# Kernel tuning notes

Hardware: AMD Instinct MI355X
Metric: run time of the kernel (lower is better)

## Reference

```python
import jax, jax.numpy as jnp
import numpy as np

WS = (2, 7, 7)   # window size (D,H,W)
SS = (1, 3, 3)   # shift size
NUM_HEADS = 12
EPS = 1e-5


def _window_partition(x, ws):
    B, D, H, W, C = x.shape
    x = x.reshape(B, D // ws[0], ws[0], H // ws[1], ws[1], W // ws[2], ws[2], C)
    return x.transpose(0, 1, 3, 5, 2, 4, 6, 7).reshape(-1, ws[0] * ws[1] * ws[2], C)


def _window_reverse(win, ws, B, D, H, W):
    x = win.reshape(B, D // ws[0], H // ws[1], W // ws[2], ws[0], ws[1], ws[2], -1)
    return x.transpose(0, 1, 4, 2, 5, 3, 6, 7).reshape(B, D, H, W, -1)


def _relative_position_index(ws):
    coords = np.stack(np.meshgrid(np.arange(ws[0]), np.arange(ws[1]), np.arange(ws[2]), indexing='ij'))
    cf = coords.reshape(3, -1)
    rel = (cf[:, :, None] - cf[:, None, :]).transpose(1, 2, 0)
    rel[:, :, 0] += ws[0] - 1
    rel[:, :, 1] += ws[1] - 1
    rel[:, :, 2] += ws[2] - 1
    rel[:, :, 0] *= (2 * ws[1] - 1) * (2 * ws[2] - 1)
    rel[:, :, 1] *= 2 * ws[2] - 1
    return rel.sum(-1)  # (N, N)


def _compute_mask(D, H, W, ws, ss):
    img = np.zeros((1, D, H, W, 1), dtype=np.float32)
    def sl(w, s):
        return [slice(-w), slice(-w, -s), slice(-s, None)] if s > 0 else [slice(None)]
    cnt = 0
    for d in sl(ws[0], ss[0]):
        for h in sl(ws[1], ss[1]):
            for w in sl(ws[2], ss[2]):
                img[:, d, h, w, :] = cnt
                cnt += 1
    # numpy window partition
    x = img.reshape(1, D // ws[0], ws[0], H // ws[1], ws[1], W // ws[2], ws[2], 1)
    mw = x.transpose(0, 1, 3, 5, 2, 4, 6, 7).reshape(-1, ws[0] * ws[1] * ws[2])
    diff = mw[:, None, :] - mw[:, :, None]
    return np.where(diff != 0, -100.0, 0.0).astype(np.float32)  # (nW, N, N)


def _layernorm(x, w, b):
    m = x.mean(-1, keepdims=True)
    v = ((x - m) ** 2).mean(-1, keepdims=True)
    return (x - m) * jax.lax.rsqrt(v + EPS) * w + b


def setup_inputs() -> dict:
    key = jax.random.key(0)
    ks = jax.random.split(key, 16)
    C = 384
    Hd = 4 * C
    nB = (2 * WS[0] - 1) * (2 * WS[1] - 1) * (2 * WS[2] - 1)
    s = lambda k, shape, f=0.02: jax.random.normal(k, shape, jnp.float32) * f
    return {
        'x': jax.random.normal(ks[0], (2, 8, 56, 56, C), jnp.float32),
        'norm1_w': jnp.ones((C,), jnp.float32), 'norm1_b': jnp.zeros((C,), jnp.float32),
        'qkv_w': s(ks[1], (3 * C, C)), 'qkv_b': jnp.zeros((3 * C,), jnp.float32),
        'rpb_table': s(ks[2], (nB, NUM_HEADS)),
        'proj_w': s(ks[3], (C, C)), 'proj_b': jnp.zeros((C,), jnp.float32),
        'norm2_w': jnp.ones((C,), jnp.float32), 'norm2_b': jnp.zeros((C,), jnp.float32),
        'fc1_w': s(ks[4], (Hd, C)), 'fc1_b': jnp.zeros((Hd,), jnp.float32),
        'fc2_w': s(ks[5], (C, Hd)), 'fc2_b': jnp.zeros((C,), jnp.float32),
    }


def reference(x, norm1_w, norm1_b, qkv_w, qkv_b, rpb_table, proj_w, proj_b,
              norm2_w, norm2_b, fc1_w, fc1_b, fc2_w, fc2_b):
    B, D, H, W, C = x.shape
    h = NUM_HEADS
    hd = C // h
    scale = hd ** -0.5
    N = WS[0] * WS[1] * WS[2]

    shortcut = x
    xn = _layernorm(x, norm1_w, norm1_b)
    # dims are exact multiples of window size -> no padding needed
    shifted = jnp.roll(xn, shift=(-SS[0], -SS[1], -SS[2]), axis=(1, 2, 3))
    xw = _window_partition(shifted, WS)  # (B_, N, C)
    B_ = xw.shape[0]

    qkv = (xw @ qkv_w.T + qkv_b).reshape(B_, N, 3, h, hd).transpose(2, 0, 3, 1, 4)
    q, k, v = qkv[0], qkv[1], qkv[2]  # (B_, h, N, hd)
    attn = jnp.einsum('bhnd,bhmd->bhnm', q * scale, k)

    rel_idx = _relative_position_index(WS)  # static numpy (N, N)
    bias = rpb_table[rel_idx.reshape(-1)].reshape(N, N, h).transpose(2, 0, 1)
    attn = attn + bias[None]

    mask = jnp.asarray(_compute_mask(D, H, W, WS, SS))  # (nW, N, N)
    nW = mask.shape[0]
    attn = attn.reshape(B_ // nW, nW, h, N, N) + mask[None, :, None]
    attn = jax.nn.softmax(attn.reshape(B_, h, N, N), axis=-1)

    out = jnp.einsum('bhnm,bhmd->bhnd', attn, v).transpose(0, 2, 1, 3).reshape(B_, N, C)
    out = out @ proj_w.T + proj_b

    xr = _window_reverse(out, WS, B, D, H, W)
    xr = jnp.roll(xr, shift=SS, axis=(1, 2, 3))
    x = shortcut + xr  # drop_path = 0

    y = _layernorm(x, norm2_w, norm2_b)
    y = jax.nn.gelu(y @ fc1_w.T + fc1_b, approximate=False) @ fc2_w.T + fc2_b
    return x + y
```

## Files before the change

### kernel.cpp

```cpp
#include <hip/hip_runtime.h>
#include <hip/hip_bf16.h>

typedef __hip_bfloat16 bf16;
typedef __attribute__((ext_vector_type(8))) short bf16x8;
typedef __attribute__((ext_vector_type(4))) float f32x4;

__device__ __forceinline__ float tof(bf16 v) { return __bfloat162float(v); }
__device__ __forceinline__ float ldf(const float* p) { return *p; }
__device__ __forceinline__ float ldf(const bf16* p) { return __bfloat162float(*p); }
__device__ __forceinline__ void stf(float* p, float v) { *p = v; }
__device__ __forceinline__ void stf(bf16* p, float v) { *p = __float2bfloat16(v); }
__device__ __forceinline__ short bfbits(float v) {
    return (short)__builtin_bit_cast(unsigned short, __float2bfloat16(v));
}

__device__ __forceinline__ void gl2lds16(const void* g, void* l) {
    __builtin_amdgcn_global_load_lds((const __attribute__((address_space(1))) void*)g,
                                     (__attribute__((address_space(3))) void*)l, 16, 0, 0);
}

constexpr int TOK   = 50176;
constexpr int CCH   = 384;
constexpr int NELEM = TOK * CCH;
constexpr int BT_N  = 8 * 12 * 98 * 112;

__device__ __forceinline__ int remap_row(int m) {
    int b_ = m / 98, n = m % 98;
    int b = b_ >> 8, wrem = b_ & 255;
    int dw = wrem >> 6, hw = (wrem >> 3) & 7, wwi = wrem & 7;
    int zd = n / 49, r = n % 49, zh = r / 7, zw = r % 7;
    int d = ((dw * 2 + zd) + 1) & 7;
    int h = hw * 7 + zh + 3; if (h >= 56) h -= 56;
    int w = wwi * 7 + zw + 3; if (w >= 56) w -= 56;
    return ((b * 8 + d) * 56 + h) * 56 + w;
}

template <bool SRC_INPUT>
__global__ __launch_bounds__(256) void ln_kernel(const void* __restrict__ srcv,
                                                 const float* __restrict__ g,
                                                 const float* __restrict__ be,
                                                 bf16* __restrict__ dst) {
    int wave = threadIdx.x >> 6, lane = threadIdx.x & 63;
    int t = blockIdx.x * 4 + wave;
    int srcRow = SRC_INPUT ? remap_row(t) : t;
    float v[6];
    float s = 0.f, ss = 0.f;
#pragma unroll
    for (int j = 0; j < 6; ++j) {
        size_t idx = (size_t)srcRow * CCH + lane + 64 * j;
        v[j] = SRC_INPUT ? ((const float*)srcv)[idx] : tof(((const bf16*)srcv)[idx]);
        s += v[j];
        ss += v[j] * v[j];
    }
#pragma unroll
    for (int off = 32; off; off >>= 1) {
        s  += __shfl_xor(s, off, 64);
        ss += __shfl_xor(ss, off, 64);
    }
    float mean = s * (1.f / 384.f);
    float var  = ss * (1.f / 384.f) - mean * mean;
    float rstd = rsqrtf(var + 1e-5f);
    bf16* q = dst + (size_t)t * CCH;
#pragma unroll
    for (int j = 0; j < 6; ++j) {
        int c = lane + 64 * j;
        stf(q + c, (v[j] - mean) * rstd * g[c] + be[c]);
    }
}

__global__ __launch_bounds__(256) void cvt_split(const float* __restrict__ w,
                                                 bf16* __restrict__ hi,
                                                 bf16* __restrict__ lo, int n) {
    int i = blockIdx.x * 256 + threadIdx.x;
    if (i >= n) return;
    float f = w[i];
    bf16 h = __float2bfloat16(f);
    hi[i] = h;
    lo[i] = __float2bfloat16(f - __bfloat162float(h));
}

__global__ __launch_bounds__(256) void bias_precomp(const float* __restrict__ rpb,
                                                    float* __restrict__ table) {
    int bid = blockIdx.x;
    int cls = bid / 12, head = bid % 12;
    int cd = (cls >> 2) & 1, ch = (cls >> 1) & 1, cw = cls & 1;
    for (int e = threadIdx.x; e < 98 * 112; e += 256) {
        int i = e / 112, j = e % 112;
        float v;
        if (j >= 98) {
            v = -1e30f;
        } else {
            int di = i / 49, ri = i % 49, hi = ri / 7, wi = ri % 7;
            int dj = j / 49, rj = j % 49, hj = rj / 7, wj = rj % 7;
            int idx = (di - dj + 1) * 169 + (hi - hj + 6) * 13 + (wi - wj + 6);
            v = rpb[(size_t)idx * 12 + head];
            int ci = (cd ? (1 + di) : 0) * 9 + (ch ? (hi < 4 ? 1 : 2) : 0) * 3 +
                     (cw ? (wi < 4 ? 1 : 2) : 0);
            int cj = (cd ? (1 + dj) : 0) * 9 + (ch ? (hj < 4 ? 1 : 2) : 0) * 3 +
                     (cw ? (wj < 4 ? 1 : 2) : 0);
            if (ci != cj) v -= 100.f;
        }
        table[(size_t)bid * 98 * 112 + e] = v;
    }
}

template <int MODE, typename CT, typename XT>
__global__ __launch_bounds__(256, 2) void gemm_mfma(const bf16* __restrict__ A, int lda,
                                                    const bf16* __restrict__ Bh,
                                                    const bf16* __restrict__ Bl, int ldb,
                                                    const float* __restrict__ bias,
                                                    CT* __restrict__ Cc, int ldc,
                                                    const XT* __restrict__ Xres,
                                                    int M, int K) {
    __shared__ short As[8192];
    __shared__ short Bhs[8192];
    __shared__ short Bls[8192];
    const int tid  = threadIdx.x;
    const int lane = tid & 63;
    const int wv   = tid >> 6;
    const int wm   = wv >> 1, wn = wv & 1;
    const int nwg  = gridDim.x * gridDim.y;
    const int orig = blockIdx.y * gridDim.x + blockIdx.x;
    const int q8 = nwg >> 3, r8 = nwg & 7;
    const int xcd = orig & 7, slot = orig >> 3;
    const int work = (xcd < r8) ? xcd * (q8 + 1) + slot
                                : r8 * (q8 + 1) + (xcd - r8) * q8 + slot;
    const int bm = (work / gridDim.x) * 128, bn = (work % gridDim.x) * 128;
    const int kb = lane >> 4, r15 = lane & 15;

    f32x4 acc[4][4] = {};

    for (int k0 = 0; k0 < K; k0 += 64) {
#pragma unroll
        for (int p = 0; p < 4; ++p) {
            const int i    = p * 256 + tid;
            const int kbb  = i >> 7;
            const int rs   = i & 127;
            const int row  = rs ^ (kbb << 1);
            const int koff = k0 + kbb * 8;
            int mrow = bm + row; if (mrow >= M) mrow = M - 1;
            const int lslot = (p * 256 + (wv << 6)) * 8;
            gl2lds16(A  + (size_t)mrow * lda + koff, &As[lslot]);
            gl2lds16(Bh + (size_t)(bn + row) * ldb + koff, &Bhs[lslot]);
            gl2lds16(Bl + (size_t)(bn + row) * ldb + koff, &Bls[lslot]);
        }
        __syncthreads();

#pragma unroll
        for (int ks = 0; ks < 2; ++ks) {
            const int kg = ks * 4 + kb;
            bf16x8 af[4];
#pragma unroll
            for (int im = 0; im < 4; ++im) {
                const int row = wm * 64 + im * 16 + r15;
                af[im] = *(const bf16x8*)&As[(kg * 128 + (row ^ (kg << 1))) * 8];
            }
#pragma unroll
            for (int in = 0; in < 4; ++in) {
                const int col = wn * 64 + in * 16 + r15;
                const int sl  = (kg * 128 + (col ^ (kg << 1))) * 8;
                const bf16x8 bh = *(const bf16x8*)&Bhs[sl];
                const bf16x8 bl = *(const bf16x8*)&Bls[sl];
#pragma unroll
                for (int im = 0; im < 4; ++im) {
                    acc[im][in] = __builtin_amdgcn_mfma_f32_16x16x32_bf16(af[im], bh, acc[im][in], 0, 0, 0);
                    acc[im][in] = __builtin_amdgcn_mfma_f32_16x16x32_bf16(af[im], bl, acc[im][in], 0, 0, 0);
                }
            }
        }
        __syncthreads();
    }

#pragma unroll
    for (int im = 0; im < 4; ++im) {
        const int mb = bm + wm * 64 + im * 16 + (lane >> 4) * 4;
#pragma unroll
        for (int in = 0; in < 4; ++in) {
            const int c = bn + wn * 64 + in * 16 + r15;
            const float bv = bias[c];
#pragma unroll
            for (int r = 0; r < 4; ++r) {
                const int m = mb + r;
                if (m >= M) continue;
                float v = acc[im][in][r] + bv;
                if (MODE == 0) {
                    stf(Cc + (size_t)m * ldc + c, v);
                } else if (MODE == 1) {
                    size_t xi = (size_t)remap_row(m) * ldc + c;
                    stf(Cc + xi, ldf(Xres + xi) + v);
                } else if (MODE == 2) {
                    stf(Cc + (size_t)m * ldc + c,
                        0.5f * v * (1.f + erff(v * 0.70710678118654752f)));
                } else {
                    size_t xi = (size_t)m * ldc + c;
                    stf(Cc + xi, ldf(Xres + xi) + v);
                }
            }
        }
    }
}

__global__ __launch_bounds__(64) void attn_kernel(const bf16* __restrict__ qkv,
                                                  const float* __restrict__ bt,
                                                  bf16* __restrict__ outw, int gbase) {
    __shared__ short Vs[112 * 32];
    __shared__ short Ps[16 * 128];
    const int bid  = blockIdx.x;
    const int head = bid % 12;
    const int brel = bid / 12;
    const int babs = gbase + brel;
    const int lane = threadIdx.x;
    const int g = lane >> 4, c15 = lane & 15;

    const size_t qbase = (size_t)brel * 98 * 1152 + head * 32;

#pragma unroll
    for (int it = 0; it < 7; ++it) {
        int c = it * 64 + lane;
        int j = c >> 2, e0 = (c & 3) * 8;
        int jc = j < 98 ? j : 97;
        *(bf16x8*)&Vs[j * 32 + e0] =
            *(const bf16x8*)(qkv + qbase + (size_t)jc * 1152 + 768 + e0);
    }
    if (lane < 32) {
        int i = lane >> 1, half = lane & 1;
        int pb = (14 + half) ^ (i & 7);
        *(bf16x8*)&Ps[i * 128 + pb * 8] = bf16x8{0, 0, 0, 0, 0, 0, 0, 0};
    }

    bf16x8 qf[7], kf[7];
#pragma unroll
    for (int t7 = 0; t7 < 7; ++t7) {
        int qi = t7 * 16 + c15; if (qi > 97) qi = 97;
        const bf16* rp = qkv + qbase + (size_t)qi * 1152 + g * 8;
        qf[t7] = *(const bf16x8*)rp;
        kf[t7] = *(const bf16x8*)(rp + 384);
    }
    __syncthreads();

    bf16x8 vb[4][2];
#pragma unroll
    for (int kb = 0; kb < 4; ++kb)
#pragma unroll
        for (int t = 0; t < 2; ++t) {
            bf16x8 f;
#pragma unroll
            for (int e = 0; e < 8; ++e) {
                int j = kb * 32 + g * 8 + e;
                int jv = j < 112 ? j : 111;
                f[e] = Vs[jv * 32 + t * 16 + c15];
            }
            vb[kb][t] = f;
        }

    const int cls = ((((babs >> 6) & 3) == 3) ? 4 : 0) |
                    ((((babs >> 3) & 7) == 7) ? 2 : 0) |
                    (((babs & 7) == 7) ? 1 : 0);
    const float* btb = bt + (size_t)(cls * 12 + head) * 98 * 112;
    const float scale = 0.17677669529663687f;

#pragma unroll 1
    for (int it = 0; it < 7; ++it) {
        f32x4 s[7];
#pragma unroll
        for (int jt = 0; jt < 7; ++jt)
            s[jt] = __builtin_amdgcn_mfma_f32_16x16x32_bf16(qf[it], kf[jt],
                                                            f32x4{0, 0, 0, 0}, 0, 0, 0);
#pragma unroll
        for (int jt = 0; jt < 7; ++jt)
#pragma unroll
            for (int r = 0; r < 4; ++r) {
                int i = it * 16 + g * 4 + r; if (i > 97) i = 97;
                s[jt][r] = fmaf(s[jt][r], scale, btb[i * 112 + jt * 16 + c15]);
            }
        float mx[4], inv[4];
#pragma unroll
        for (int r = 0; r < 4; ++r) {
            float m = s[0][r];
#pragma unroll
            for (int jt = 1; jt < 7; ++jt) m = fmaxf(m, s[jt][r]);
#pragma unroll
            for (int off = 8; off; off >>= 1) m = fmaxf(m, __shfl_xor(m, off, 64));
            mx[r] = m;
        }
#pragma unroll
        for (int jt = 0; jt < 7; ++jt)
#pragma unroll
            for (int r = 0; r < 4; ++r) s[jt][r] = __expf(s[jt][r] - mx[r]);
#pragma unroll
        for (int r = 0; r < 4; ++r) {
            float t = 0.f;
#pragma unroll
            for (int jt = 0; jt < 7; ++jt) t += s[jt][r];
#pragma unroll
            for (int off = 8; off; off >>= 1) t += __shfl_xor(t, off, 64);
            inv[r] = 1.f / t;
        }
#pragma unroll
        for (int jt = 0; jt < 7; ++jt)
#pragma unroll
            for (int r = 0; r < 4; ++r) {
                int i = g * 4 + r;
                int j = jt * 16 + c15;
                int pj = ((((j >> 3) ^ (i & 7)) << 3)) | (j & 7);
                Ps[i * 128 + pj] = bfbits(s[jt][r]);
            }
        f32x4 o[2] = {f32x4{0, 0, 0, 0}, f32x4{0, 0, 0, 0}};
#pragma unroll
        for (int kb = 0; kb < 4; ++kb) {
            int pb = (kb * 4 + g) ^ (c15 & 7);
            bf16x8 pa = *(const bf16x8*)&Ps[c15 * 128 + pb * 8];
#pragma unroll
            for (int t = 0; t < 2; ++t)
                o[t] = __builtin_amdgcn_mfma_f32_16x16x32_bf16(pa, vb[kb][t], o[t], 0, 0, 0);
        }
#pragma unroll
        for (int t = 0; t < 2; ++t)
#pragma unroll
            for (int r = 0; r < 4; ++r) {
                int i = it * 16 + g * 4 + r;
                if (i < 98)
                    stf(outw + ((size_t)babs * 98 + i) * 384 + head * 32 + t * 16 + c15,
                        o[t][r] * inv[r]);
            }
    }
}

extern "C" void kernel_launch(void* const* d_in, const int* in_sizes, int n_in,
                              void* d_out, int out_size, void* d_ws, size_t ws_size,
                              hipStream_t stream) {
    const float* x      = (const float*)d_in[0];
    const float* n1w    = (const float*)d_in[1];
    const float* n1b    = (const float*)d_in[2];
    const float* qkv_w  = (const float*)d_in[3];
    const float* qkv_b  = (const float*)d_in[4];
    const float* rpb    = (const float*)d_in[5];
    const float* proj_w = (const float*)d_in[6];
    const float* proj_b = (const float*)d_in[7];
    const float* n2w    = (const float*)d_in[8];
    const float* n2b    = (const float*)d_in[9];
    const float* fc1_w  = (const float*)d_in[10];
    const float* fc1_b  = (const float*)d_in[11];
    const float* fc2_w  = (const float*)d_in[12];
    const float* fc2_b  = (const float*)d_in[13];

    bf16*  aout = (bf16*)d_out;
    float* btab = (float*)((char*)d_out + (size_t)NELEM * 2);
    bf16*  xn2  = (bf16*)((char*)d_out + (size_t)NELEM * 2);
    float* fout = (float*)d_out;

    constexpr int QKV_WN  = 1152 * 384;
    constexpr int PROJ_WN = 384 * 384;
    constexpr int FC1_WN  = 1536 * 384;
    constexpr int FC2_WN  = 384 * 1536;
    bf16* qh   = (bf16*)d_ws;
    bf16* ql   = qh  + QKV_WN;
    bf16* ph   = ql  + QKV_WN;
    bf16* pl   = ph  + PROJ_WN;
    bf16* f1h  = pl  + PROJ_WN;
    bf16* f1l  = f1h + FC1_WN;
    bf16* f2h  = f1l + FC1_WN;
    bf16* f2l  = f2h + FC2_WN;
    bf16* rA   = f2l + FC2_WN;
    bf16* rC   = rA + (size_t)NELEM;
    size_t used    = (size_t)((char*)rC - (char*)d_ws);
    size_t rCbytes = (ws_size > used) ? ws_size - used : 0;

    cvt_split<<<(QKV_WN  + 255) / 256, 256, 0, stream>>>(qkv_w,  qh,  ql,  QKV_WN);
    cvt_split<<<(PROJ_WN + 255) / 256, 256, 0, stream>>>(proj_w, ph,  pl,  PROJ_WN);
    cvt_split<<<(FC1_WN  + 255) / 256, 256, 0, stream>>>(fc1_w,  f1h, f1l, FC1_WN);
    cvt_split<<<(FC2_WN  + 255) / 256, 256, 0, stream>>>(fc2_w,  f2h, f2l, FC2_WN);
    bias_precomp<<<96, 256, 0, stream>>>(rpb, btab);

    int W = 512;
    while (W > 1 && (size_t)W * 98 * 1152 * 2 > rCbytes) W >>= 1;
    int nqg = 512 / W;
    int ngm = 1;
    while (ngm < 1024 && (size_t)(TOK / ngm) * 1536 * 2 > rCbytes) ngm <<= 1;
    int Mt = TOK / ngm;

    dim3 blk(256);

    ln_kernel<true><<<dim3(TOK / 4), blk, 0, stream>>>(x, n1w, n1b, rA);
    for (int g = 0; g < nqg; ++g) {
        int Mg = W * 98;
        gemm_mfma<0, bf16, float><<<dim3(1152 / 128, (Mg + 127) / 128), blk, 0, stream>>>(
            rA + (size_t)g * Mg * 384, 384, qh, ql, 384, qkv_b,
            rC, 1152, (const float*)nullptr, Mg, 384);
        attn_kernel<<<dim3(W * 12), dim3(64), 0, stream>>>(rC, btab, aout, g * W);
    }
    gemm_mfma<1, bf16, float><<<dim3(384 / 128, TOK / 128), blk, 0, stream>>>(
        aout, 384, ph, pl, 384, proj_b, rA, 384, x, TOK, 384);
    ln_kernel<false><<<dim3(TOK / 4), blk, 0, stream>>>(rA, n2w, n2b, xn2);
    for (int g = 0; g < ngm; ++g) {
        size_t off = (size_t)g * Mt * 384;
        gemm_mfma<2, bf16, float><<<dim3(1536 / 128, (Mt + 127) / 128), blk, 0, stream>>>(
            xn2 + off, 384, f1h, f1l, 384, fc1_b, rC, 1536, (const float*)nullptr, Mt, 384);
        gemm_mfma<4, float, bf16><<<dim3(384 / 128, (Mt + 127) / 128), blk, 0, stream>>>(
            rC, 1536, f2h, f2l, 1536, fc2_b, fout + off, 384, rA + off, Mt, 1536);
    }
}
```

Before: 1.196 ms.

## Double-buffer GEMM LDS tiles with BK=32 and use tanh-form GELU

The GEMM main loop now splits the LDS tiles into two 32-wide K buffers. It issues the global-to-LDS loads for the next K slice before running the MFMAs on the current one, so memory latency overlaps compute and one barrier per step is dropped. Separately, the fused GELU epilogue replaces the exact erf with a tanh approximation built from __expf and a hardware reciprocal. That makes the epilogue cheaper but departs slightly from the exact-erf GELU the reference specifies.

```diff
diff --git a/kernel.cpp b/kernel.cpp
--- a/kernel.cpp
+++ b/kernel.cpp
@@ -112,9 +112,9 @@
                                                     CT* __restrict__ Cc, int ldc,
                                                     const XT* __restrict__ Xres,
                                                     int M, int K) {
-    __shared__ short As[8192];
-    __shared__ short Bhs[8192];
-    __shared__ short Bls[8192];
+    __shared__ short As[2][4096];
+    __shared__ short Bhs[2][4096];
+    __shared__ short Bls[2][4096];
     const int tid  = threadIdx.x;
     const int lane = tid & 63;
     const int wv   = tid >> 6;
@@ -130,46 +130,55 @@
 
     f32x4 acc[4][4] = {};
 
-    for (int k0 = 0; k0 < K; k0 += 64) {
-#pragma unroll
-        for (int p = 0; p < 4; ++p) {
-            const int i    = p * 256 + tid;
-            const int kbb  = i >> 7;
-            const int rs   = i & 127;
-            const int row  = rs ^ (kbb << 1);
-            const int koff = k0 + kbb * 8;
-            int mrow = bm + row; if (mrow >= M) mrow = M - 1;
-            const int lslot = (p * 256 + (wv << 6)) * 8;
-            gl2lds16(A  + (size_t)mrow * lda + koff, &As[lslot]);
-            gl2lds16(Bh + (size_t)(bn + row) * ldb + koff, &Bhs[lslot]);
-            gl2lds16(Bl + (size_t)(bn + row) * ldb + koff, &Bls[lslot]);
+    const int i0   = tid, i1 = 256 + tid;
+    const int kbb0 = i0 >> 7, kbb1 = i1 >> 7;
+    const int row0 = (i0 & 127) ^ (kbb0 << 1);
+    const int row1 = (i1 & 127) ^ (kbb1 << 1);
+    int mrow0 = bm + row0; if (mrow0 >= M) mrow0 = M - 1;
+    int mrow1 = bm + row1; if (mrow1 >= M) mrow1 = M - 1;
+    const int ls0 = (0 * 256 + (wv << 6)) * 8;
+    const int ls1 = (1 * 256 + (wv << 6)) * 8;
+
+#define STAGE(buf, k0)                                                              \
+    do {                                                                            \
+        gl2lds16(A  + (size_t)mrow0 * lda + (k0) + kbb0 * 8, &As[buf][ls0]);        \
+        gl2lds16(Bh + (size_t)(bn + row0) * ldb + (k0) + kbb0 * 8, &Bhs[buf][ls0]); \
+        gl2lds16(Bl + (size_t)(bn + row0) * ldb + (k0) + kbb0 * 8, &Bls[buf][ls0]); \
+        gl2lds16(A  + (size_t)mrow1 * lda + (k0) + kbb1 * 8, &As[buf][ls1]);        \
+        gl2lds16(Bh + (size_t)(bn + row1) * ldb + (k0) + kbb1 * 8, &Bhs[buf][ls1]); \
+        gl2lds16(Bl + (size_t)(bn + row1) * ldb + (k0) + kbb1 * 8, &Bls[buf][ls1]); \
+    } while (0)
+
+    STAGE(0, 0);
+    __syncthreads();
+
+    const int nk = K >> 5;
+    int cur = 0;
+    for (int t = 0; t < nk; ++t) {
+        if (t + 1 < nk) STAGE(cur ^ 1, (t + 1) * 32);
+
+        bf16x8 af[4];
+#pragma unroll
+        for (int im = 0; im < 4; ++im) {
+            const int row = wm * 64 + im * 16 + r15;
+            af[im] = *(const bf16x8*)&As[cur][(kb * 128 + (row ^ (kb << 1))) * 8];
+        }
+#pragma unroll
+        for (int in = 0; in < 4; ++in) {
+            const int col = wn * 64 + in * 16 + r15;
+            const int sl  = (kb * 128 + (col ^ (kb << 1))) * 8;
+            const bf16x8 bh = *(const bf16x8*)&Bhs[cur][sl];
+            const bf16x8 bl = *(const bf16x8*)&Bls[cur][sl];
+#pragma unroll
+            for (int im = 0; im < 4; ++im) {
+                acc[im][in] = __builtin_amdgcn_mfma_f32_16x16x32_bf16(af[im], bh, acc[im][in], 0, 0, 0);
+                acc[im][in] = __builtin_amdgcn_mfma_f32_16x16x32_bf16(af[im], bl, acc[im][in], 0, 0, 0);
+            }
         }
         __syncthreads();
-
-#pragma unroll
-        for (int ks = 0; ks < 2; ++ks) {
-            const int kg = ks * 4 + kb;
-            bf16x8 af[4];
-#pragma unroll
-            for (int im = 0; im < 4; ++im) {
-                const int row = wm * 64 + im * 16 + r15;
-                af[im] = *(const bf16x8*)&As[(kg * 128 + (row ^ (kg << 1))) * 8];
-            }
-#pragma unroll
-            for (int in = 0; in < 4; ++in) {
-                const int col = wn * 64 + in * 16 + r15;
-                const int sl  = (kg * 128 + (col ^ (kg << 1))) * 8;
-                const bf16x8 bh = *(const bf16x8*)&Bhs[sl];
-                const bf16x8 bl = *(const bf16x8*)&Bls[sl];
-#pragma unroll
-                for (int im = 0; im < 4; ++im) {
-                    acc[im][in] = __builtin_amdgcn_mfma_f32_16x16x32_bf16(af[im], bh, acc[im][in], 0, 0, 0);
-                    acc[im][in] = __builtin_amdgcn_mfma_f32_16x16x32_bf16(af[im], bl, acc[im][in], 0, 0, 0);
-                }
-            }
-        }
-        __syncthreads();
-    }
+        cur ^= 1;
+    }
+#undef STAGE
 
 #pragma unroll
     for (int im = 0; im < 4; ++im) {
@@ -189,8 +198,10 @@
                     size_t xi = (size_t)remap_row(m) * ldc + c;
                     stf(Cc + xi, ldf(Xres + xi) + v);
                 } else if (MODE == 2) {
-                    stf(Cc + (size_t)m * ldc + c,
-                        0.5f * v * (1.f + erff(v * 0.70710678118654752f)));
+                    float u  = v * fmaf(0.0356774081f, v * v, 0.7978845608f);
+                    float e  = __expf(2.f * u);
+                    float th = 1.f - 2.f * __builtin_amdgcn_rcpf(e + 1.f);
+                    stf(Cc + (size_t)m * ldc + c, 0.5f * v * (1.f + th));
                 } else {
                     size_t xi = (size_t)m * ldc + c;
                     stf(Cc + xi, ldf(Xres + xi) + v);
```

Result: no change. 1.173 ms (-1.9%).
